# Kernel optimization log

Measured on AMD Instinct MI355X. Metric: run time of the kernel, lower is better.

## Reference

```python
import jax, jax.numpy as jnp
import numpy as np

EMB_DIM = 512
QKV_DIM = 512
NUM_HEADS = 8
HEAD_DIM = QKV_DIM // NUM_HEADS  # 64
BATCH = 4
SEQLEN = 2048


def _gaussian_orthogonal_random_matrix(rng, nb_rows, nb_cols):
    # Matches torch gaussian_orthogonal_random_matrix with scaling=0.
    blocks = []
    n_full = nb_rows // nb_cols
    for _ in range(n_full):
        q, _ = np.linalg.qr(rng.standard_normal((nb_cols, nb_cols)))
        blocks.append(q.T)
    rem = nb_rows - n_full * nb_cols
    if rem > 0:
        q, _ = np.linalg.qr(rng.standard_normal((nb_cols, nb_cols)))
        blocks.append(q.T[:rem])
    mat = np.concatenate(blocks, axis=0)
    mult = np.linalg.norm(rng.standard_normal((nb_rows, nb_cols)), axis=1)
    return (mult[:, None] * mat).astype(np.float32)


def setup_inputs() -> dict:
    key = jax.random.key(0)
    ks = jax.random.split(key, 9)
    s = 0.02
    inp = {
        'x': jax.random.normal(ks[0], (BATCH, SEQLEN, EMB_DIM), jnp.float32),
        'Wq': jax.random.normal(ks[1], (EMB_DIM, QKV_DIM), jnp.float32) * s,
        'bq': jnp.zeros((QKV_DIM,), jnp.float32),
        'Wk': jax.random.normal(ks[2], (EMB_DIM, QKV_DIM), jnp.float32) * s,
        'bk': jnp.zeros((QKV_DIM,), jnp.float32),
        'Wv': jax.random.normal(ks[3], (EMB_DIM, QKV_DIM), jnp.float32) * s,
        'bv': jnp.zeros((QKV_DIM,), jnp.float32),
        'Wo': jax.random.normal(ks[4], (QKV_DIM, EMB_DIM), jnp.float32) * s,
        'bo': jnp.zeros((EMB_DIM,), jnp.float32),
        'proj': jnp.asarray(_gaussian_orthogonal_random_matrix(
            np.random.default_rng(0), QKV_DIM, HEAD_DIM)),  # (m=qkv_dim, head_dim)
    }
    return inp


def _split_heads(x):
    b, s, _ = x.shape
    return x.reshape(b, s, NUM_HEADS, HEAD_DIM).transpose(0, 2, 1, 3)  # (b,h,s,d)


def _softmax_kernel(data, proj, is_query, eps=1e-4):
    # data: (b,h,n,d); proj: (m,d)
    d = data.shape[-1]
    dn = d ** -0.25                       # data normalizer
    ratio = proj.shape[0] ** -0.5         # m^{-1/2}
    data_dash = jnp.einsum('bhnd,md->bhnm', dn * data, proj)
    diag = jnp.sum(data * data, axis=-1, keepdims=True) * (0.5 * dn * dn)
    if is_query:
        m = jax.lax.stop_gradient(jnp.max(data_dash, axis=-1, keepdims=True))
    else:
        m = jax.lax.stop_gradient(jnp.max(data_dash, axis=(-1, -2), keepdims=True))
    return ratio * (jnp.exp(data_dash - diag - m) + eps)


def _linear_attn(q, k, v):
    # q,k: (b,h,n,m); v: (b,h,n,d)
    k_cumsum = jnp.sum(k, axis=-2)                                  # (b,h,m)
    d_inv = 1.0 / jnp.einsum('bhnm,bhm->bhn', q, k_cumsum)          # (b,h,n)
    context = jnp.einsum('bhnm,bhnd->bhmd', k, v)                   # (b,h,m,d)
    return jnp.einsum('bhmd,bhnm,bhn->bhnd', context, q, d_inv)


def reference(x, Wq, bq, Wk, bk, Wv, bv, Wo, bo, proj):
    q = _split_heads(x @ Wq + bq)
    k = _split_heads(x @ Wk + bk)
    v = _split_heads(x @ Wv + bv)
    qp = _softmax_kernel(q, proj, is_query=True)
    kp = _softmax_kernel(k, proj, is_query=False)
    out = _linear_attn(qp, kp, v)                                   # (b,h,n,d)
    b, h, n, d = out.shape
    out = out.transpose(0, 2, 1, 3).reshape(b, n, h * d)            # combine heads
    return out @ Wo + bo
```

## Files before the change

### kernel.cpp

```cpp
#include <hip/hip_runtime.h>

typedef unsigned short u16;
typedef unsigned int   u32;
typedef __attribute__((ext_vector_type(8))) short bf16x8;
typedef __attribute__((ext_vector_type(4))) short s16x4;
typedef __attribute__((ext_vector_type(4))) float f32x4;

#define MFMA16(a,b,c) __builtin_amdgcn_mfma_f32_16x16x32_bf16((a),(b),(c),0,0,0)

#define SOFT_BAR_LG() do{ asm volatile("s_waitcnt lgkmcnt(0)" ::: "memory"); \
  __builtin_amdgcn_s_barrier(); __builtin_amdgcn_sched_barrier(0); }while(0)
#define SOFT_BAR_VM(N) do{ asm volatile("s_waitcnt vmcnt(" #N ") lgkmcnt(0)" ::: "memory"); \
  __builtin_amdgcn_s_barrier(); __builtin_amdgcn_sched_barrier(0); }while(0)

__device__ __forceinline__ float bf2f(u16 u){ return __uint_as_float(((u32)u)<<16); }
__device__ __forceinline__ u16 f2bf(float f){
  u32 u = __float_as_uint(f);
  return (u16)((u + 0x7fffu + ((u>>16)&1u)) >> 16);
}
__device__ __forceinline__ u32 encf(float f){ u32 u=__float_as_uint(f); return (u&0x80000000u)? ~u : (u|0x80000000u); }
__device__ __forceinline__ float decf(u32 u){ return (u&0x80000000u)? __uint_as_float(u&0x7fffffffu) : __uint_as_float(~u); }

__device__ __forceinline__ void async_lds16(u16* lds, const u16* g){
  __builtin_amdgcn_global_load_lds((const __attribute__((address_space(1))) void*)g,
                                   (__attribute__((address_space(3))) void*)lds,
                                   16, 0, 0);
}

template<int ROWS>
__device__ __forceinline__ void stage64(u16* dst, const u16* src, int srcStride, int tid){
  #pragma unroll
  for (int u=tid; u<ROWS*8; u+=256){
    int r=u>>3, c=(u&7)<<3;
    *(int4*)&dst[r*72+c] = *(const int4*)&src[(size_t)r*srcStride + c];
  }
}

__global__ __launch_bounds__(256) void k_setup(u32* kmaxEnc, u16* projS,
    const float* __restrict__ proj, const float* __restrict__ x, u16* __restrict__ xb,
    const float* s0, const float* s1, const float* s2, const float* s3,
    u16* d0, u16* d1, u16* d2, u16* d3)
{
  int bid=blockIdx.x, tid=threadIdx.x;
  if (bid < 1024){
    int z = bid>>8, t = bid&255;
    const float* src = z==0?s0:(z==1?s1:(z==2?s2:s3));
    u16* dst         = z==0?d0:(z==1?d1:(z==2?d2:d3));
    __shared__ u16 tl[32][34];
    int c0=(t&15)*32, r0=(t>>4)*32;
    for (int u=tid; u<1024; u+=256){ int r=u>>5, c=u&31; tl[r][c]=f2bf(src[(size_t)(r0+r)*512 + c0+c]); }
    __syncthreads();
    for (int u=tid; u<1024; u+=256){ int c=u>>5, r=u&31; dst[(size_t)(c0+c)*512 + r0+r]=tl[r][c]; }
  } else {
    int i = (bid-1024)*256 + tid;
    int st = 256*256;
    for (int j=i; j<32; j+=st) kmaxEnc[j]=0u;
    const float dn = 0.35355339059327373f;
    for (int j=i; j<512*64; j+=st) projS[j] = f2bf(dn*proj[j]);
    for (int j=i; j<524288; j+=st){
      float4 a = *(const float4*)&x[(size_t)j*8];
      float4 b = *(const float4*)&x[(size_t)j*8+4];
      u16 tmp[8] = {f2bf(a.x),f2bf(a.y),f2bf(a.z),f2bf(a.w),
                    f2bf(b.x),f2bf(b.y),f2bf(b.z),f2bf(b.w)};
      *(int4*)&xb[(size_t)j*8] = *(const int4*)tmp;
    }
  }
}

__global__ __launch_bounds__(256) void k_prep(const u16* __restrict__ vB, u16* __restrict__ vT,
    float* __restrict__ vsum, const u16* __restrict__ kB, float* __restrict__ diagK)
{
  int bid=blockIdx.x, tid=threadIdx.x;
  if (bid < 4096){
    int xx=bid&1, y=(bid>>1)&63, bh=bid>>7;
    int b=bh>>3, h=bh&7;
    int dd0=xx*32, n0=y*32;
    __shared__ u16 t[32][34];
    const u16* s = vB + (size_t)(b*2048)*512 + h*64;
    for (int u=tid; u<1024; u+=256){ int r=u>>5, c=u&31; t[r][c]=s[(size_t)(n0+r)*512 + dd0+c]; }
    __syncthreads();
    u16* d = vT + (size_t)bh*64*2048;
    for (int u=tid; u<1024; u+=256){ int c=u>>5, r=u&31; d[(size_t)(dd0+c)*2048 + n0+r]=t[r][c]; }
  } else if (bid < 4128){
    int bh=bid-4096; int b=bh>>3, h=bh&7;
    int d=tid&63, part=tid>>6;
    const u16* src = vB + (size_t)(b*2048 + part*512)*512 + h*64 + d;
    float s=0.f;
    for (int n=0;n<512;++n) s += bf2f(src[(size_t)n*512]);
    __shared__ float red[256];
    red[tid]=s; __syncthreads();
    if (part==0) vsum[bh*64+d]=red[d]+red[64+d]+red[128+d]+red[192+d];
  } else {
    int idx=bid-4128;
    int bh=idx&31, seg=idx>>5;
    int b=bh>>3, h=bh&7;
    int part=tid&7;
    const u16* base = kB + (size_t)(b*2048 + seg*256)*512 + h*64 + part*8;
    for (int n0=0; n0<256; n0+=32){
      int n = n0 + (tid>>3);
      bf16x8 v = *(const bf16x8*)&base[(size_t)n*512];
      float sq=0.f;
      #pragma unroll
      for (int j=0;j<8;++j){ float f=bf2f((u16)v[j]); sq+=f*f; }
      sq += __shfl_xor(sq,1,64); sq += __shfl_xor(sq,2,64); sq += __shfl_xor(sq,4,64);
      if (part==0) diagK[(size_t)bh*2048 + seg*256 + n] = 0.0625f*sq;
    }
  }
}

template<bool OF32>
__global__ __launch_bounds__(256) void k_gemm2(const u16* __restrict__ A,
    const u16* BT0, const u16* BT1, const u16* BT2,
    const float* b0, const float* b1, const float* b2,
    void* O0, void* O1, void* O2)
{
  int z = blockIdx.z;
  const u16* BT    = z==0?BT0:(z==1?BT1:BT2);
  const float* bias= z==0?b0 :(z==1?b1 :b2 );
  void* Ov         = z==0?O0 :(z==1?O1 :O2 );
  int bm = blockIdx.x*128, bn = blockIdx.y*64;
  __shared__ u16 sA[128*64];
  __shared__ u16 sB[64*64];
  int tid=threadIdx.x, w=tid>>6, lane=tid&63;
  int lr = lane>>3, lc = (lane&7)*8;
  f32x4 acc[8] = {};
  for (int kk=0; kk<512; kk+=64){
    __syncthreads();
    #pragma unroll
    for (int i=0;i<4;++i){
      int idx = w*4+i;
      async_lds16(&sA[idx*512], A + (size_t)(bm + idx*8 + lr)*512 + kk + lc);
    }
    #pragma unroll
    for (int i=0;i<2;++i){
      int idx = w*2+i;
      async_lds16(&sB[idx*512], BT + (size_t)(bn + idx*8 + lr)*512 + kk + lc);
    }
    __syncthreads();
    int fr = lane&15, kb=(lane>>4)*8;
    #pragma unroll
    for (int rt=0; rt<2; ++rt){
      int ar = (w*2+rt)*16 + fr;
      #pragma unroll
      for (int ct=0; ct<4; ++ct){
        int br = ct*16 + fr;
        #pragma unroll
        for (int kc=0; kc<2; ++kc){
          bf16x8 av = *(const bf16x8*)&sA[ar*64 + kc*32 + kb];
          bf16x8 bv = *(const bf16x8*)&sB[br*64 + kc*32 + kb];
          acc[rt*4+ct] = MFMA16(av,bv,acc[rt*4+ct]);
        }
      }
    }
  }
  int colg = lane&15, rowg=(lane>>4)*4;
  #pragma unroll
  for (int rt=0; rt<2; ++rt){
    #pragma unroll
    for (int ct=0; ct<4; ++ct){
      int col = bn + ct*16 + colg;
      float bv = bias[col];
      #pragma unroll
      for (int j=0;j<4;++j){
        int row = bm + (w*2+rt)*16 + rowg + j;
        if constexpr (OF32) ((float*)Ov)[(size_t)row*512 + col] = acc[rt*4+ct][j] + bv;
        else                ((u16*) Ov)[(size_t)row*512 + col] = f2bf(acc[rt*4+ct][j] + bv);
      }
    }
  }
}

__global__ __launch_bounds__(256) void k_kpctx3(const u16* __restrict__ kB, const u16* __restrict__ projS,
    const u16* __restrict__ vT, const float* __restrict__ diagK,
    float* __restrict__ ctxPT, float* __restrict__ kcsP, u32* __restrict__ kmaxEnc)
{
  int h=blockIdx.x, y=blockIdx.y, b=blockIdx.z;
  int mblk = y&7, s = y>>3;
  int bh=b*8+h;
  int m0 = mblk*64;
  __shared__ __align__(16) u16 sK[128*72];
  __shared__ __align__(16) u16 sV[64*136];
  __shared__ __align__(16) u16 sP[64*72];
  __shared__ __align__(16) u16 sT[64*136];
  __shared__ float sDg[128];
  __shared__ float red[4];
  __shared__ float sRed[4][64];
  int tid=threadIdx.x, w=tid>>6, lane=tid&63;
  int fr=lane&15, kbg=lane>>4, kb=kbg*8, rowg=kbg*4;
  stage64<64>(sP, projS + m0*64, 64, tid);
  f32x4 accc[4]={};
  float sSm[4]={0.f,0.f,0.f,0.f};
  float lm=-3.0e38f;
  const u16* gK = kB + (size_t)(b*2048 + s*1024)*512 + h*64;
  const u16* gV = vT + (size_t)bh*64*2048 + s*1024;
  const float* gD = diagK + (size_t)bh*2048 + s*1024;
  int4 pK[4], pV[4]; float4 pD={0.f,0.f,0.f,0.f};
  #pragma unroll
  for (int i=0;i<4;++i){ int u=tid+i*256; int r=u>>3,c=(u&7)<<3; pK[i]=*(const int4*)&gK[(size_t)r*512 + c]; }
  #pragma unroll
  for (int i=0;i<4;++i){ int u=tid+i*256; int r=u>>4,c=(u&15)<<3; pV[i]=*(const int4*)&gV[(size_t)r*2048 + c]; }
  if (tid<32) pD = *(const float4*)&gD[tid*4];
  for (int nc=0; nc<8; ++nc){
    #pragma unroll
    for (int i=0;i<4;++i){ int u=tid+i*256; int r=u>>3,c=(u&7)<<3; *(int4*)&sK[r*72+c]=pK[i]; }
    #pragma unroll
    for (int i=0;i<4;++i){ int u=tid+i*256; int r=u>>4,c=(u&15)<<3; *(int4*)&sV[r*136+c]=pV[i]; }
    if (tid<32) *(float4*)&sDg[tid*4] = pD;
    __syncthreads();
    if (nc<7){
      #pragma unroll
      for (int i=0;i<4;++i){ int u=tid+i*256; int r=u>>3,c=(u&7)<<3; pK[i]=*(const int4*)&gK[(size_t)((nc+1)*128+r)*512 + c]; }
      #pragma unroll
      for (int i=0;i<4;++i){ int u=tid+i*256; int r=u>>4,c=(u&15)<<3; pV[i]=*(const int4*)&gV[(size_t)r*2048 + (nc+1)*128 + c]; }
      if (tid<32) pD = *(const float4*)&gD[(nc+1)*128 + tid*4];
    }
    f32x4 facc[2][4];
    #pragma unroll
    for (int rt=0;rt<2;++rt){
      int ar=(w*2+rt)*16+fr;
      #pragma unroll
      for (int mt=0;mt<4;++mt){
        f32x4 a={0.f,0.f,0.f,0.f};
        a=MFMA16(*(const bf16x8*)&sK[ar*72+kb],    *(const bf16x8*)&sP[(mt*16+fr)*72+kb],    a);
        a=MFMA16(*(const bf16x8*)&sK[ar*72+32+kb], *(const bf16x8*)&sP[(mt*16+fr)*72+32+kb], a);
        facc[rt][mt]=a;
        lm=fmaxf(lm, fmaxf(fmaxf(a[0],a[1]),fmaxf(a[2],a[3])));
      }
    }
    #pragma unroll
    for (int rt=0;rt<2;++rt){
      int nl=(w*2+rt)*16+rowg;
      #pragma unroll
      for (int mt=0;mt<4;++mt){
        int ml=mt*16+fr;
        s16x4 pk;
        #pragma unroll
        for (int j=0;j<4;++j){
          float vk = __expf(facc[rt][mt][j]-sDg[nl+j]);
          u16 us = f2bf(vk);
          pk[j]=(short)us;
          sSm[mt] += bf2f(us);
        }
        *(s16x4*)&sT[ml*136+nl]=pk;
      }
    }
    __syncthreads();
    int am=w*16+fr;
    #pragma unroll
    for (int ct=0;ct<4;++ct){
      #pragma unroll
      for (int ks=0;ks<4;++ks){
        accc[ct]=MFMA16(*(const bf16x8*)&sT[am*136+ks*32+kb],
                        *(const bf16x8*)&sV[(ct*16+fr)*136+ks*32+kb], accc[ct]);
      }
    }
    __syncthreads();
  }
  #pragma unroll
  for (int mt=0;mt<4;++mt){
    float t=sSm[mt];
    t += __shfl_xor(t,16,64); t += __shfl_xor(t,32,64);
    if (kbg==0) sRed[w][mt*16+fr]=t;
  }
  #pragma unroll
  for (int m2=1;m2<64;m2<<=1) lm=fmaxf(lm,__shfl_xor(lm,m2,64));
  if (lane==0) red[w]=lm;
  float* sTf = (float*)sT;
  int mloc = w*16+rowg;
  #pragma unroll
  for (int ct=0;ct<4;++ct){
    #pragma unroll
    for (int j=0;j<4;++j) sTf[(ct*16+fr)*68 + mloc + j] = accc[ct][j];
  }
  __syncthreads();
  if (tid==0) atomicMax(&kmaxEnc[bh], encf(fmaxf(fmaxf(red[0],red[1]),fmaxf(red[2],red[3]))));
  if (tid<64) kcsP[(size_t)(s*32+bh)*512 + m0 + tid] =
      sRed[0][tid]+sRed[1][tid]+sRed[2][tid]+sRed[3][tid];
  for (int u=tid; u<1024; u+=256){
    int r=u>>4, c=(u&15)*4;
    *(float4*)&ctxPT[((size_t)(s*32+bh)*64 + r)*512 + m0 + c] = *(const float4*)&sTf[r*68+c];
  }
}

__global__ __launch_bounds__(256) void k_comb2(const float* __restrict__ ctxPT, u16* __restrict__ ctxT,
    const float* __restrict__ kcsP, float* __restrict__ kcs,
    float* __restrict__ ctxsum, float* __restrict__ kcssum)
{
  int bh=blockIdx.x, dblk=blockIdx.y;
  int tid=threadIdx.x;
  int d0=dblk*8;
  __shared__ float sDsum[8];
  __shared__ float sKsum[256];
  if (tid<8) sDsum[tid]=0.f;
  __syncthreads();
  const float* p0 = ctxPT + ((size_t)bh*64 + d0)*512;
  const float* p1 = ctxPT + ((size_t)(32+bh)*64 + d0)*512;
  u16* o = ctxT + ((size_t)bh*64 + d0)*512;
  for (int u=tid; u<1024; u+=256){
    int r=u>>7, c=(u&127)*4;
    float4 a=*(const float4*)&p0[(size_t)r*512+c];
    float4 bq=*(const float4*)&p1[(size_t)r*512+c];
    float vx=a.x+bq.x, vy=a.y+bq.y, vz=a.z+bq.z, vw=a.w+bq.w;
    u16 t[4]={f2bf(vx),f2bf(vy),f2bf(vz),f2bf(vw)};
    *(int2*)&o[(size_t)r*512+c] = *(const int2*)t;
    atomicAdd(&sDsum[r], bf2f(t[0])+bf2f(t[1])+bf2f(t[2])+bf2f(t[3]));
  }
  float tpart=0.f;
  if (dblk==0){
    for (int u=tid; u<512; u+=256){
      float t = kcsP[(size_t)bh*512+u] + kcsP[(size_t)(32+bh)*512+u];
      kcs[(size_t)bh*512+u]=t;
      tpart += t;
    }
  }
  sKsum[tid]=tpart;
  __syncthreads();
  if (tid<8) ctxsum[bh*64 + d0 + tid] = sDsum[tid];
  if (dblk==0 && tid<64){
    float a=sKsum[tid]+sKsum[tid+64]+sKsum[tid+128]+sKsum[tid+192];
    #pragma unroll
    for (int m2=1;m2<64;m2<<=1) a += __shfl_xor(a,m2,64);
    if (tid==0) kcssum[bh]=a;
  }
}

__global__ __launch_bounds__(256) void k_qpout3(const u16* __restrict__ qB, const u16* __restrict__ projS,
    const float* __restrict__ kcs, const u16* __restrict__ ctxT,
    const float* __restrict__ ctxsum, const float* __restrict__ kcssum,
    const float* __restrict__ vsum, const u32* __restrict__ kmaxEnc,
    u16* __restrict__ outc)
{
  int h=blockIdx.x, chunk=blockIdx.y, b=blockIdx.z;
  int bh=b*8+h;
  int t0 = b*2048 + chunk*64;
  __shared__ u16 sP[2][64*64];
  __shared__ u16 sCt[64*64];
  __shared__ u16 qpL[64*72];
  __shared__ float sK[512];
  __shared__ float diag[64];
  int tid=threadIdx.x, w=tid>>6, lane=tid&63;
  int fr=lane&15, kbg=lane>>4, kb=kbg*8, rowg=kbg*4;
  int lr=lane>>3, lgl=((lane&7)^lr)*8;
  int sw=fr&7;
  bf16x8 qf[2];
  #pragma unroll
  for (int kc=0;kc<2;++kc)
    qf[kc] = *(const bf16x8*)&qB[(size_t)(t0 + w*16 + fr)*512 + h*64 + kc*32 + kb];
  {
    float ssum=0.f;
    #pragma unroll
    for (int kc=0;kc<2;++kc)
      #pragma unroll
      for (int j=0;j<8;++j){ float f=bf2f((u16)qf[kc][j]); ssum+=f*f; }
    ssum += __shfl_xor(ssum,16,64); ssum += __shfl_xor(ssum,32,64);
    if (lane<16) diag[w*16 + fr] = 0.0625f*ssum;
  }
  for (int u=tid; u<512; u+=256) sK[u] = kcs[(size_t)bh*512 + u];
  const u16* gcB = ctxT + (size_t)bh*64*512;
  #pragma unroll
  for (int i=0;i<2;++i){
    int idx = w*2+i;
    async_lds16(&sP[0][idx*512], projS + (size_t)(idx*8+lr)*64 + lgl);
  }
  f32x4 acc2[4]={};
  float mx[4], dp[4], rs[4];
  #pragma unroll
  for (int j=0;j<4;++j){ mx[j]=-3.0e38f; dp[j]=0.f; rs[j]=0.f; }
  SOFT_BAR_VM(0);
  for (int mc=0; mc<8; ++mc){
    int cur = mc&1;
    #pragma unroll
    for (int i=0;i<2;++i){
      int idx = w*2+i;
      async_lds16(&sCt[idx*512], gcB + (size_t)(idx*8+lr)*512 + mc*64 + lgl);
    }
    if (mc<7){
      const u16* gp = projS + (mc+1)*64*64;
      #pragma unroll
      for (int i=0;i<2;++i){
        int idx = w*2+i;
        async_lds16(&sP[cur^1][idx*512], gp + (size_t)(idx*8+lr)*64 + lgl);
      }
    }
    f32x4 facc[4];
    #pragma unroll
    for (int mt=0;mt<4;++mt){
      f32x4 a={0.f,0.f,0.f,0.f};
      #pragma unroll
      for (int kc=0;kc<2;++kc){
        bf16x8 bv = *(const bf16x8*)&sP[cur][(mt*16+fr)*64 + (((kc*4+kbg)^sw)<<3)];
        a = MFMA16(qf[kc], bv, a);
      }
      facc[mt]=a;
    }
    #pragma unroll
    for (int mt=0;mt<4;++mt){
      #pragma unroll
      for (int j=0;j<4;++j){
        int rl = w*16 + rowg + j;
        mx[j] = fmaxf(mx[j], facc[mt][j]);
        float vq = __expf(facc[mt][j] - diag[rl]);
        u16 us = f2bf(vq);
        qpL[rl*72 + mt*16 + fr] = us;
        float uf = bf2f(us);
        dp[j] += uf*sK[mc*64 + mt*16 + fr];
        rs[j] += uf;
      }
    }
    if (mc<7) { SOFT_BAR_VM(2); } else { SOFT_BAR_VM(0); }
    #pragma unroll
    for (int ct=0;ct<4;++ct){
      #pragma unroll
      for (int kc=0;kc<2;++kc){
        bf16x8 av = *(const bf16x8*)&qpL[(w*16+fr)*72 + kc*32 + kb];
        bf16x8 bv = *(const bf16x8*)&sCt[(ct*16+fr)*64 + (((kc*4+kbg)^sw)<<3)];
        acc2[ct] = MFMA16(av,bv,acc2[ct]);
      }
    }
    if (mc<7) { SOFT_BAR_VM(0); }
  }
  #pragma unroll
  for (int j=0;j<4;++j){
    #pragma unroll
    for (int s=1;s<16;s<<=1){
      dp[j] += __shfl_xor(dp[j],s,64);
      rs[j] += __shfl_xor(rs[j],s,64);
      mx[j]  = fmaxf(mx[j], __shfl_xor(mx[j],s,64));
    }
  }
  float mk  = decf(kmaxEnc[bh]);
  float emk = __expf(mk);
  float Ssum = kcssum[bh];
  const float eps=1e-4f;
  float emq[4];
  #pragma unroll
  for (int j=0;j<4;++j) emq[j]=__expf(mx[j]);
  #pragma unroll
  for (int ct=0;ct<4;++ct){
    int d = ct*16 + fr;
    float cs = ctxsum[bh*64 + d];
    float vs = vsum[bh*64 + d];
    #pragma unroll
    for (int j=0;j<4;++j){
      float eq = emq[j];
      float numer = acc2[ct][j] + eps*(emk*vs*rs[j] + eq*cs + eps*eq*emk*512.0f*vs);
      float den   = dp[j]       + eps*(emk*2048.0f*rs[j] + eq*Ssum + eps*eq*emk*512.0f*2048.0f);
      int row = t0 + w*16 + rowg + j;
      outc[(size_t)row*512 + h*64 + d] = f2bf(numer/den);
    }
  }
}

extern "C" void kernel_launch(void* const* d_in, const int* in_sizes, int n_in,
                              void* d_out, int out_size, void* d_ws, size_t ws_size,
                              hipStream_t stream)
{
  (void)in_sizes; (void)n_in; (void)out_size; (void)ws_size;
  const float* x    = (const float*)d_in[0];
  const float* Wq   = (const float*)d_in[1];
  const float* bq   = (const float*)d_in[2];
  const float* Wk   = (const float*)d_in[3];
  const float* bk   = (const float*)d_in[4];
  const float* Wv   = (const float*)d_in[5];
  const float* bv   = (const float*)d_in[6];
  const float* Wo   = (const float*)d_in[7];
  const float* bo   = (const float*)d_in[8];
  const float* proj = (const float*)d_in[9];

  char* w = (char*)d_ws;
  size_t off=0;
  auto alloc=[&](size_t bytes)->char*{ char* p=w+off; off=(off+bytes+255)&~(size_t)255; return p; };
  u16*  xb   = (u16*)alloc(8192ull*512*2);
  u16*  qB   = (u16*)alloc(8192ull*512*2);
  u16*  kBf  = (u16*)alloc(8192ull*512*2);
  u16*  vB   = (u16*)alloc(8192ull*512*2);
  u16*  vT   = (u16*)alloc(32ull*64*2048*2);
  u16*  WqT  = (u16*)alloc(512ull*512*2);
  u16*  WkT  = (u16*)alloc(512ull*512*2);
  u16*  WvT  = (u16*)alloc(512ull*512*2);
  u16*  WoT  = (u16*)alloc(512ull*512*2);
  u16*  projS= (u16*)alloc(512ull*64*2);
  u16*  ctxT = (u16*)alloc(32ull*64*512*2);
  float* ctxPT=(float*)alloc(2ull*32*64*512*4);
  float* kcs = (float*)alloc(32ull*512*4);
  float* kcsP= (float*)alloc(2ull*32*512*4);
  float* diagK=(float*)alloc(32ull*2048*4);
  u32*  kmx  = (u32*)alloc(256);
  float* ctxs= (float*)alloc(32ull*64*4);
  float* kcss= (float*)alloc(32ull*4);
  float* vsm = (float*)alloc(32ull*64*4);
  u16*  outc = kBf;

  dim3 TB(256);
  k_setup<<<dim3(1280),TB,0,stream>>>(kmx,projS,proj,x,xb, Wq,Wk,Wv,Wo, WqT,WkT,WvT,WoT);
  k_gemm2<false><<<dim3(64,8,3),TB,0,stream>>>(xb, WqT,WkT,WvT, bq,bk,bv, qB,kBf,vB);
  k_prep<<<dim3(4384),TB,0,stream>>>(vB, vT, vsm, kBf, diagK);
  k_kpctx3<<<dim3(8,16,4),TB,0,stream>>>(kBf, projS, vT, diagK, ctxPT, kcsP, kmx);
  k_comb2<<<dim3(32,8),TB,0,stream>>>(ctxPT, ctxT, kcsP, kcs, ctxs, kcss);
  k_qpout3<<<dim3(8,32,4),TB,0,stream>>>(qB, projS, kcs, ctxT, ctxs, kcss, vsm, kmx, outc);
  k_gemm2<true><<<dim3(64,8,1),TB,0,stream>>>(outc, WoT,WoT,WoT, bo,bo,bo,
                                              d_out,d_out,d_out);
}
```

Baseline: 145.0 us.

## Split K-context kernel into four sequence chunks with async LDS double-buffering

The key-feature/context kernel now splits the sequence into four 512-row chunks instead of two, doubling the grid. Its register-staged K/V loads are replaced by async global-to-LDS loads into XOR-swizzled double buffers, and diag values are preloaded into registers. Per-iteration work drops to 64 rows, and the combine kernel now sums four partials instead of two. The aim is more parallelism and better latency hiding with less LDS. The cost is larger partial buffers and more reduction traffic in the combine step.

```diff
diff --git a/kernel.cpp b/kernel.cpp
--- a/kernel.cpp
+++ b/kernel.cpp
@@ -170,7 +170,7 @@
   }
 }
 
-__global__ __launch_bounds__(256) void k_kpctx3(const u16* __restrict__ kB, const u16* __restrict__ projS,
+__global__ __launch_bounds__(256) void k_kpctx6(const u16* __restrict__ kB, const u16* __restrict__ projS,
     const u16* __restrict__ vT, const float* __restrict__ diagK,
     float* __restrict__ ctxPT, float* __restrict__ kcsP, u32* __restrict__ kmaxEnc)
 {
@@ -178,84 +178,97 @@
   int mblk = y&7, s = y>>3;
   int bh=b*8+h;
   int m0 = mblk*64;
-  __shared__ __align__(16) u16 sK[128*72];
-  __shared__ __align__(16) u16 sV[64*136];
   __shared__ __align__(16) u16 sP[64*72];
-  __shared__ __align__(16) u16 sT[64*136];
-  __shared__ float sDg[128];
+  __shared__ __align__(16) u16 poolKV[3*4096];
+  __shared__ __align__(16) u16 sT[64*72];
+  __shared__ float sRed[4][64];
   __shared__ float red[4];
-  __shared__ float sRed[4][64];
+  u16* sK0 = poolKV;
+  u16* sK1 = poolKV + 4096;
+  u16* sV  = poolKV + 8192;
   int tid=threadIdx.x, w=tid>>6, lane=tid&63;
   int fr=lane&15, kbg=lane>>4, kb=kbg*8, rowg=kbg*4;
+  int lr=lane>>3, lgl=((lane&7)^lr)*8;
+  int sw=fr&7;
+  const u16* gK = kB + (size_t)(b*2048 + s*512)*512 + h*64;
+  const u16* gV = vT + (size_t)bh*64*2048 + s*512;
+  const float* gD = diagK + (size_t)bh*2048 + s*512 + w*16 + rowg;
   stage64<64>(sP, projS + m0*64, 64, tid);
+  float4 pD[8];
+  #pragma unroll
+  for (int mc=0;mc<8;++mc) pD[mc] = *(const float4*)&gD[mc*64];
+  #pragma unroll
+  for (int i=0;i<2;++i){
+    int idx = w*2+i;
+    async_lds16(&sK0[idx*512], gK + (size_t)(idx*8+lr)*512 + lgl);
+  }
   f32x4 accc[4]={};
   float sSm[4]={0.f,0.f,0.f,0.f};
   float lm=-3.0e38f;
-  const u16* gK = kB + (size_t)(b*2048 + s*1024)*512 + h*64;
-  const u16* gV = vT + (size_t)bh*64*2048 + s*1024;
-  const float* gD = diagK + (size_t)bh*2048 + s*1024;
-  int4 pK[4], pV[4]; float4 pD={0.f,0.f,0.f,0.f};
-  #pragma unroll
-  for (int i=0;i<4;++i){ int u=tid+i*256; int r=u>>3,c=(u&7)<<3; pK[i]=*(const int4*)&gK[(size_t)r*512 + c]; }
-  #pragma unroll
-  for (int i=0;i<4;++i){ int u=tid+i*256; int r=u>>4,c=(u&15)<<3; pV[i]=*(const int4*)&gV[(size_t)r*2048 + c]; }
-  if (tid<32) pD = *(const float4*)&gD[tid*4];
-  for (int nc=0; nc<8; ++nc){
-    #pragma unroll
-    for (int i=0;i<4;++i){ int u=tid+i*256; int r=u>>3,c=(u&7)<<3; *(int4*)&sK[r*72+c]=pK[i]; }
-    #pragma unroll
-    for (int i=0;i<4;++i){ int u=tid+i*256; int r=u>>4,c=(u&15)<<3; *(int4*)&sV[r*136+c]=pV[i]; }
-    if (tid<32) *(float4*)&sDg[tid*4] = pD;
-    __syncthreads();
-    if (nc<7){
-      #pragma unroll
-      for (int i=0;i<4;++i){ int u=tid+i*256; int r=u>>3,c=(u&7)<<3; pK[i]=*(const int4*)&gK[(size_t)((nc+1)*128+r)*512 + c]; }
-      #pragma unroll
-      for (int i=0;i<4;++i){ int u=tid+i*256; int r=u>>4,c=(u&15)<<3; pV[i]=*(const int4*)&gV[(size_t)r*2048 + (nc+1)*128 + c]; }
-      if (tid<32) pD = *(const float4*)&gD[(nc+1)*128 + tid*4];
-    }
-    f32x4 facc[2][4];
-    #pragma unroll
-    for (int rt=0;rt<2;++rt){
-      int ar=(w*2+rt)*16+fr;
-      #pragma unroll
-      for (int mt=0;mt<4;++mt){
-        f32x4 a={0.f,0.f,0.f,0.f};
-        a=MFMA16(*(const bf16x8*)&sK[ar*72+kb],    *(const bf16x8*)&sP[(mt*16+fr)*72+kb],    a);
-        a=MFMA16(*(const bf16x8*)&sK[ar*72+32+kb], *(const bf16x8*)&sP[(mt*16+fr)*72+32+kb], a);
-        facc[rt][mt]=a;
-        lm=fmaxf(lm, fmaxf(fmaxf(a[0],a[1]),fmaxf(a[2],a[3])));
-      }
-    }
-    #pragma unroll
-    for (int rt=0;rt<2;++rt){
-      int nl=(w*2+rt)*16+rowg;
+  SOFT_BAR_VM(0);
+  #pragma unroll
+  for (int mc=0; mc<8; ++mc){
+    u16* sKc = (mc&1) ? sK1 : sK0;
+    u16* sKn = (mc&1) ? sK0 : sK1;
+    #pragma unroll
+    for (int i=0;i<2;++i){
+      int idx = w*2+i;
+      async_lds16(&sV[idx*512], gV + (size_t)(idx*8+lr)*2048 + mc*64 + lgl);
+    }
+    if (mc<7){
+      #pragma unroll
+      for (int i=0;i<2;++i){
+        int idx = w*2+i;
+        async_lds16(&sKn[idx*512], gK + (size_t)((mc+1)*64 + idx*8+lr)*512 + lgl);
+      }
+    }
+    int ar = w*16 + fr;
+    f32x4 facc[4];
+    #pragma unroll
+    for (int mt=0;mt<4;++mt){
+      f32x4 a={0.f,0.f,0.f,0.f};
+      #pragma unroll
+      for (int kc=0;kc<2;++kc){
+        bf16x8 av = *(const bf16x8*)&sKc[ar*64 + (((kc*4+kbg)^sw)<<3)];
+        bf16x8 bv = *(const bf16x8*)&sP[(mt*16+fr)*72 + kc*32 + kb];
+        a = MFMA16(av,bv,a);
+      }
+      facc[mt]=a;
+      lm=fmaxf(lm, fmaxf(fmaxf(a[0],a[1]),fmaxf(a[2],a[3])));
+    }
+    {
+      int nl = w*16 + rowg;
       #pragma unroll
       for (int mt=0;mt<4;++mt){
         int ml=mt*16+fr;
         s16x4 pk;
         #pragma unroll
         for (int j=0;j<4;++j){
-          float vk = __expf(facc[rt][mt][j]-sDg[nl+j]);
+          float vk = __expf(facc[mt][j]-pD[mc][j]);
           u16 us = f2bf(vk);
           pk[j]=(short)us;
           sSm[mt] += bf2f(us);
         }
-        *(s16x4*)&sT[ml*136+nl]=pk;
-      }
-    }
-    __syncthreads();
-    int am=w*16+fr;
-    #pragma unroll
-    for (int ct=0;ct<4;++ct){
-      #pragma unroll
-      for (int ks=0;ks<4;++ks){
-        accc[ct]=MFMA16(*(const bf16x8*)&sT[am*136+ks*32+kb],
-                        *(const bf16x8*)&sV[(ct*16+fr)*136+ks*32+kb], accc[ct]);
-      }
-    }
-    __syncthreads();
-  }
+        *(s16x4*)&sT[ml*72+nl]=pk;
+      }
+      (void)nl;
+    }
+    if (mc<7) { SOFT_BAR_VM(2); } else { SOFT_BAR_VM(0); }
+    {
+      int am=w*16+fr;
+      #pragma unroll
+      for (int ct=0;ct<4;++ct){
+        #pragma unroll
+        for (int kc=0;kc<2;++kc){
+          bf16x8 av = *(const bf16x8*)&sT[am*72 + kc*32 + kb];
+          bf16x8 bv = *(const bf16x8*)&sV[(ct*16+fr)*64 + (((kc*4+kbg)^sw)<<3)];
+          accc[ct] = MFMA16(av,bv,accc[ct]);
+        }
+      }
+    }
+    if (mc<7) { SOFT_BAR_VM(0); }
+  }
+  __syncthreads();
   #pragma unroll
   for (int mt=0;mt<4;++mt){
     float t=sSm[mt];
@@ -265,7 +278,7 @@
   #pragma unroll
   for (int m2=1;m2<64;m2<<=1) lm=fmaxf(lm,__shfl_xor(lm,m2,64));
   if (lane==0) red[w]=lm;
-  float* sTf = (float*)sT;
+  float* sTf = (float*)poolKV;
   int mloc = w*16+rowg;
   #pragma unroll
   for (int ct=0;ct<4;++ct){
@@ -282,7 +295,7 @@
   }
 }
 
-__global__ __launch_bounds__(256) void k_comb2(const float* __restrict__ ctxPT, u16* __restrict__ ctxT,
+__global__ __launch_bounds__(256) void k_comb4(const float* __restrict__ ctxPT, u16* __restrict__ ctxT,
     const float* __restrict__ kcsP, float* __restrict__ kcs,
     float* __restrict__ ctxsum, float* __restrict__ kcssum)
 {
@@ -293,22 +306,25 @@
   __shared__ float sKsum[256];
   if (tid<8) sDsum[tid]=0.f;
   __syncthreads();
-  const float* p0 = ctxPT + ((size_t)bh*64 + d0)*512;
-  const float* p1 = ctxPT + ((size_t)(32+bh)*64 + d0)*512;
   u16* o = ctxT + ((size_t)bh*64 + d0)*512;
   for (int u=tid; u<1024; u+=256){
     int r=u>>7, c=(u&127)*4;
-    float4 a=*(const float4*)&p0[(size_t)r*512+c];
-    float4 bq=*(const float4*)&p1[(size_t)r*512+c];
-    float vx=a.x+bq.x, vy=a.y+bq.y, vz=a.z+bq.z, vw=a.w+bq.w;
-    u16 t[4]={f2bf(vx),f2bf(vy),f2bf(vz),f2bf(vw)};
+    float4 a={0.f,0.f,0.f,0.f};
+    #pragma unroll
+    for (int s=0;s<4;++s){
+      float4 p=*(const float4*)&ctxPT[((size_t)(s*32+bh)*64 + d0+r)*512 + c];
+      a.x+=p.x; a.y+=p.y; a.z+=p.z; a.w+=p.w;
+    }
+    u16 t[4]={f2bf(a.x),f2bf(a.y),f2bf(a.z),f2bf(a.w)};
     *(int2*)&o[(size_t)r*512+c] = *(const int2*)t;
     atomicAdd(&sDsum[r], bf2f(t[0])+bf2f(t[1])+bf2f(t[2])+bf2f(t[3]));
   }
   float tpart=0.f;
   if (dblk==0){
     for (int u=tid; u<512; u+=256){
-      float t = kcsP[(size_t)bh*512+u] + kcsP[(size_t)(32+bh)*512+u];
+      float t=0.f;
+      #pragma unroll
+      for (int s=0;s<4;++s) t += kcsP[(size_t)(s*32+bh)*512+u];
       kcs[(size_t)bh*512+u]=t;
       tpart += t;
     }
@@ -481,9 +497,9 @@
   u16*  WoT  = (u16*)alloc(512ull*512*2);
   u16*  projS= (u16*)alloc(512ull*64*2);
   u16*  ctxT = (u16*)alloc(32ull*64*512*2);
-  float* ctxPT=(float*)alloc(2ull*32*64*512*4);
+  float* ctxPT=(float*)alloc(4ull*32*64*512*4);
   float* kcs = (float*)alloc(32ull*512*4);
-  float* kcsP= (float*)alloc(2ull*32*512*4);
+  float* kcsP= (float*)alloc(4ull*32*512*4);
   float* diagK=(float*)alloc(32ull*2048*4);
   u32*  kmx  = (u32*)alloc(256);
   float* ctxs= (float*)alloc(32ull*64*4);
@@ -495,8 +511,8 @@
   k_setup<<<dim3(1280),TB,0,stream>>>(kmx,projS,proj,x,xb, Wq,Wk,Wv,Wo, WqT,WkT,WvT,WoT);
   k_gemm2<false><<<dim3(64,8,3),TB,0,stream>>>(xb, WqT,WkT,WvT, bq,bk,bv, qB,kBf,vB);
   k_prep<<<dim3(4384),TB,0,stream>>>(vB, vT, vsm, kBf, diagK);
-  k_kpctx3<<<dim3(8,16,4),TB,0,stream>>>(kBf, projS, vT, diagK, ctxPT, kcsP, kmx);
-  k_comb2<<<dim3(32,8),TB,0,stream>>>(ctxPT, ctxT, kcsP, kcs, ctxs, kcss);
+  k_kpctx6<<<dim3(8,32,4),TB,0,stream>>>(kBf, projS, vT, diagK, ctxPT, kcsP, kmx);
+  k_comb4<<<dim3(32,8),TB,0,stream>>>(ctxPT, ctxT, kcsP, kcs, ctxs, kcss);
   k_qpout3<<<dim3(8,32,4),TB,0,stream>>>(qB, projS, kcs, ctxT, ctxs, kcss, vsm, kmx, outc);
   k_gemm2<true><<<dim3(64,8,1),TB,0,stream>>>(outc, WoT,WoT,WoT, bo,bo,bo,
                                               d_out,d_out,d_out);
```

Result: faster. 132.5 us (-8.6%).
